# Kernel optimization log

Measured on AMD Instinct MI355X. Metric: run time of the kernel, lower is better.

The kernel has to match this reference:

```python
import jax, jax.numpy as jnp
import numpy as np

QMIN = 0.0
QMAX = 255.0  # uint8, asymmetric


def fake_quant(x, scale, zp):
    # asymmetric uint8 fake-quantization: q = clamp(round(x/s + zp), 0, 255); dq = (q - zp) * s
    s = scale.reshape(())
    z = zp.reshape(())
    q = jnp.clip(jnp.round(x / s + z), QMIN, QMAX)
    return (q - z) * s


def setup_inputs() -> dict:
    key = jax.random.key(0)
    k1, k2 = jax.random.split(key)
    B, M, K, N = 4, 2048, 4096, 4096
    x1 = jax.random.normal(k1, (B, M, K), dtype=jnp.float32)
    x2 = jax.random.normal(k2, (B, K, N), dtype=jnp.float32)
    # realistic learned per-tensor scale / zero-point for ~N(0,1) data over uint8 range
    x1_scale = jnp.full((1,), 8.0 / 255.0, dtype=jnp.float32)
    x1_zp = jnp.full((1,), 128.0, dtype=jnp.float32)
    x2_scale = jnp.full((1,), 8.0 / 255.0, dtype=jnp.float32)
    x2_zp = jnp.full((1,), 128.0, dtype=jnp.float32)
    return {"x1": x1, "x2": x2, "x1_scale": x1_scale, "x1_zp": x1_zp,
            "x2_scale": x2_scale, "x2_zp": x2_zp}


def reference(x1, x2, x1_scale, x1_zp, x2_scale, x2_zp):
    q1 = fake_quant(x1, x1_scale, x1_zp)  # [B, M, K]
    q2 = fake_quant(x2, x2_scale, x2_zp)  # [B, K, N]
    return jnp.matmul(q1, q2)             # [B, M, N]
```

## Files before the change

### kernel.cpp

```cpp
#include <hip/hip_runtime.h>
#include <stdint.h>

typedef int v4i __attribute__((ext_vector_type(4)));

#define GLOBAL_AS __attribute__((address_space(1)))
#define LDS_AS __attribute__((address_space(3)))

__device__ __forceinline__ int quant1(float x, float s, float z, int zi) {
    float q = rintf(x / s + z);
    q = fminf(fmaxf(q, 0.0f), 255.0f);
    return (int)q - zi;
}

__device__ __forceinline__ unsigned qpack4(float4 v, float s, float z, int zi) {
    unsigned q0 = (unsigned)(quant1(v.x, s, z, zi) & 255);
    unsigned q1 = (unsigned)(quant1(v.y, s, z, zi) & 255);
    unsigned q2 = (unsigned)(quant1(v.z, s, z, zi) & 255);
    unsigned q3 = (unsigned)(quant1(v.w, s, z, zi) & 255);
    return q0 | (q1 << 8) | (q2 << 16) | (q3 << 24);
}

__global__ __launch_bounds__(256) void quant_lin(const float* __restrict__ x,
                                                 int8_t* __restrict__ out,
                                                 const float* __restrict__ sp,
                                                 const float* __restrict__ zp,
                                                 long n16) {
    float s = sp[0], z = zp[0];
    int zi = (int)rintf(z);
    long i = (long)blockIdx.x * 256 + threadIdx.x;
    if (i >= n16) return;
    const float4* xv = (const float4*)x;
    uint4 w;
    w.x = qpack4(xv[i * 4 + 0], s, z, zi);
    w.y = qpack4(xv[i * 4 + 1], s, z, zi);
    w.z = qpack4(xv[i * 4 + 2], s, z, zi);
    w.w = qpack4(xv[i * 4 + 3], s, z, zi);
    ((uint4*)out)[i] = w;
}

__global__ __launch_bounds__(256) void quant_bt(const float* __restrict__ x,
                                                int8_t* __restrict__ out,
                                                const float* __restrict__ sp,
                                                const float* __restrict__ zp) {
    constexpr int K = 4096, N = 4096;
    float s = sp[0], z = zp[0];
    int zi = (int)rintf(z);
    size_t bin = (size_t)blockIdx.z * K * N;
    int tid = threadIdx.x;
    int bk = tid >> 4;
    int bn = tid & 15;
    int k0 = blockIdx.y * 64, n0 = blockIdx.x * 64;
    __shared__ unsigned lds[64][17];
    unsigned o0 = 0, o1 = 0, o2 = 0, o3 = 0;
#pragma unroll
    for (int r = 0; r < 4; ++r) {
        float4 v = *(const float4*)(x + bin + (size_t)(k0 + bk * 4 + r) * N + n0 + bn * 4);
        o0 |= (unsigned)(quant1(v.x, s, z, zi) & 255) << (r * 8);
        o1 |= (unsigned)(quant1(v.y, s, z, zi) & 255) << (r * 8);
        o2 |= (unsigned)(quant1(v.z, s, z, zi) & 255) << (r * 8);
        o3 |= (unsigned)(quant1(v.w, s, z, zi) & 255) << (r * 8);
    }
    lds[bn * 4 + 0][bk] = o0;
    lds[bn * 4 + 1][bk] = o1;
    lds[bn * 4 + 2][bk] = o2;
    lds[bn * 4 + 3][bk] = o3;
    __syncthreads();
    int nl = tid >> 2, ch = tid & 3;
    uint4 w;
    w.x = lds[nl][ch * 4 + 0];
    w.y = lds[nl][ch * 4 + 1];
    w.z = lds[nl][ch * 4 + 2];
    w.w = lds[nl][ch * 4 + 3];
    *(uint4*)(out + bin + (size_t)(n0 + nl) * K + k0 + ch * 16) = w;
}

__global__ __launch_bounds__(512, 1) void gemm_i8(const int8_t* __restrict__ A,
                                                  const int8_t* __restrict__ Bt,
                                                  float* __restrict__ C,
                                                  const float* __restrict__ sp1,
                                                  const float* __restrict__ sp2) {
    constexpr int M = 2048, N = 4096, K = 4096;
    constexpr int BM = 256, BN = 256, BK = 64;
    constexpr int NBN = N / BN;

    extern __shared__ char smem[];

    int b = blockIdx.z;
    const int8_t* Ab = A + (size_t)b * M * K;
    const int8_t* Bb = Bt + (size_t)b * N * K;
    float* Cb = C + (size_t)b * M * N;

    int nwg = gridDim.x;
    int wg = blockIdx.x;
    wg = (wg & 7) * (nwg >> 3) + (wg >> 3);
    int by = wg / NBN, bx = wg % NBN;
    int m0 = by * BM, n0 = bx * BN;

    int tid = threadIdx.x;
    int lane = tid & 63, wid = tid >> 6;
    int wr = wid >> 2, wc = wid & 3;
    int l15 = lane & 15, cb = lane >> 4;

    int row0 = tid >> 2, cc0 = tid & 3;
    int sw0 = cc0 ^ ((row0 >> 1) & 3);
    const size_t PSTEP = (size_t)128 * K;
    const int8_t* pA = Ab + (size_t)(m0 + row0) * K + sw0 * 16;
    const int8_t* pB = Bb + (size_t)(n0 + row0) * K + sw0 * 16;
    const unsigned dbase = (unsigned)tid * 16;

    int ra = wr * 128 + l15;
    int aoff0 = ra * 64 + ((cb ^ ((ra >> 1) & 3)) * 16);
    int rb_ = wc * 64 + l15;
    int boff0 = 16384 + rb_ * 64 + ((cb ^ ((rb_ >> 1) & 3)) * 16);

    v4i zero = {0, 0, 0, 0};
    v4i acc[8][4];
#pragma unroll
    for (int m = 0; m < 8; ++m)
#pragma unroll
        for (int n = 0; n < 4; ++n) acc[m][n] = zero;

    v4i fA0[8], fB0[4], fA1[8], fB1[4];

#define ISSUE(S)                                                                        \
    {                                                                                   \
        char* d = smem + (S)*32768 + dbase;                                             \
        __builtin_amdgcn_global_load_lds((const GLOBAL_AS void*)pA,                     \
                                         (LDS_AS void*)d, 16, 0, 0);                    \
        __builtin_amdgcn_global_load_lds((const GLOBAL_AS void*)(pA + PSTEP),           \
                                         (LDS_AS void*)(d + 8192), 16, 0, 0);           \
        __builtin_amdgcn_global_load_lds((const GLOBAL_AS void*)pB,                     \
                                         (LDS_AS void*)(d + 16384), 16, 0, 0);          \
        __builtin_amdgcn_global_load_lds((const GLOBAL_AS void*)(pB + PSTEP),           \
                                         (LDS_AS void*)(d + 24576), 16, 0, 0);          \
        pA += BK;                                                                       \
        pB += BK;                                                                       \
    }

#define RD(S, fa, fb)                                                                   \
    {                                                                                   \
        const char* rbp = smem + (S)*32768;                                             \
        _Pragma("unroll") for (int n = 0; n < 4; ++n)                                   \
            fb[n] = *(const v4i*)(rbp + boff0 + n * 1024);                              \
        _Pragma("unroll") for (int m = 0; m < 8; ++m)                                   \
            fa[m] = *(const v4i*)(rbp + aoff0 + m * 1024);                              \
    }

#define MM(fa, fb)                                                                      \
    {                                                                                   \
        __builtin_amdgcn_s_setprio(1);                                                  \
        _Pragma("unroll") for (int m = 0; m < 8; ++m)                                   \
            _Pragma("unroll") for (int n = 0; n < 4; ++n)                               \
                acc[m][n] = __builtin_amdgcn_mfma_i32_16x16x64_i8(fa[m], fb[n],         \
                                                                  acc[m][n], 0, 0, 0);  \
        __builtin_amdgcn_s_setprio(0);                                                  \
    }

#define SGB3()                                                                          \
    __builtin_amdgcn_sched_group_barrier(0x30, 4, 0);                                   \
    __builtin_amdgcn_sched_group_barrier(0x100, 12, 0);                                 \
    __builtin_amdgcn_sched_group_barrier(0x8, 32, 0);

#define STEP(SI, SR, CA, CB, NA, NB)                                                    \
    {                                                                                   \
        ISSUE(SI);                                                                      \
        RD(SR, NA, NB);                                                                 \
        MM(CA, CB);                                                                     \
        SGB3();                                                                         \
        asm volatile("s_waitcnt vmcnt(4)" ::: "memory");                                \
        __builtin_amdgcn_s_barrier();                                                   \
        asm volatile("" ::: "memory");                                                  \
    }

    ISSUE(0);
    ISSUE(1);
    ISSUE(2);
    asm volatile("s_waitcnt vmcnt(4)" ::: "memory");
    __builtin_amdgcn_s_barrier();
    asm volatile("" ::: "memory");
    RD(0, fA0, fB0);

    for (int it = 0; it < 15; ++it) {
        STEP(3, 1, fA0, fB0, fA1, fB1)
        STEP(0, 2, fA1, fB1, fA0, fB0)
        STEP(1, 3, fA0, fB0, fA1, fB1)
        STEP(2, 0, fA1, fB1, fA0, fB0)
    }
    STEP(3, 1, fA0, fB0, fA1, fB1)
    {
        RD(2, fA0, fB0);
        MM(fA1, fB1);
        asm volatile("s_waitcnt vmcnt(0)" ::: "memory");
        __builtin_amdgcn_s_barrier();
        asm volatile("" ::: "memory");
    }
    RD(3, fA1, fB1);
    MM(fA0, fB0);
    MM(fA1, fB1);

    float sc = sp1[0] * sp2[0];
    int r0 = cb * 4;
#pragma unroll
    for (int m = 0; m < 8; ++m) {
#pragma unroll
        for (int n = 0; n < 4; ++n) {
            float* p = Cb + (size_t)(m0 + wr * 128 + m * 16 + r0) * N +
                       (n0 + wc * 64 + n * 16 + l15);
#pragma unroll
            for (int r = 0; r < 4; ++r) p[(size_t)r * N] = sc * (float)acc[m][n][r];
        }
    }
#undef ISSUE
#undef RD
#undef MM
#undef SGB3
#undef STEP
}

extern "C" void kernel_launch(void* const* d_in, const int* in_sizes, int n_in,
                              void* d_out, int out_size, void* d_ws, size_t ws_size,
                              hipStream_t stream) {
    const float* x1 = (const float*)d_in[0];
    const float* x2 = (const float*)d_in[1];
    const float* s1 = (const float*)d_in[2];
    const float* z1 = (const float*)d_in[3];
    const float* s2 = (const float*)d_in[4];
    const float* z2 = (const float*)d_in[5];
    float* out = (float*)d_out;

    const int B = 4, M = 2048, K = 4096, N = 4096;
    const size_t ASZ = (size_t)B * M * K;
    const size_t BSZ = (size_t)B * K * N;
    dim3 blk(256);

    static int lds_attr_set = 0;
    if (!lds_attr_set) {
        (void)hipFuncSetAttribute((const void*)gemm_i8,
                                  hipFuncAttributeMaxDynamicSharedMemorySize, 131072);
        lds_attr_set = 1;
    }

    if (ws_size >= ASZ + BSZ) {
        int8_t* Aq = (int8_t*)d_ws;
        int8_t* Bq = Aq + ASZ;
        long n16 = (long)(ASZ / 16);
        quant_lin<<<dim3((unsigned)(n16 / 256)), blk, 0, stream>>>(x1, Aq, s1, z1, n16);
        quant_bt<<<dim3(N / 64, K / 64, B), blk, 0, stream>>>(x2, Bq, s2, z2);
        gemm_i8<<<dim3((M / 256) * (N / 256), 1, B), dim3(512), 131072, stream>>>(
            Aq, Bq, out, s1, s2);
    } else {
        const size_t AB = (size_t)M * K, BB = (size_t)K * N;
        int8_t* Aq = (int8_t*)d_ws;
        int8_t* Bq = Aq + AB;
        for (int b = 0; b < B; ++b) {
            long n16 = (long)(AB / 16);
            quant_lin<<<dim3((unsigned)(n16 / 256)), blk, 0, stream>>>(x1 + (size_t)b * AB, Aq, s1, z1, n16);
            quant_bt<<<dim3(N / 64, K / 64, 1), blk, 0, stream>>>(x2 + (size_t)b * BB, Bq, s2, z2);
            gemm_i8<<<dim3((M / 256) * (N / 256), 1, 1), dim3(512), 131072, stream>>>(
                Aq, Bq, out + (size_t)b * M * N, s1, s2);
        }
    }
}
```

Baseline: 250.2 us.

## Deepen GEMM pipeline to five LDS stages and remap grid for XCD locality

The int8 GEMM grows from four to five LDS buffers (160 KB of dynamic LDS), so one more global load stage is in flight, and the wait threshold rises to keep two stages outstanding. The main loop is restructured into a 10-step unrolled cycle with a matching drain sequence. The batched launch becomes a flat 512-block grid whose mapping gives each XCD a contiguous region of one batch, to improve L2 reuse of A and B tiles. The deeper pipeline is meant to hide memory latency better, at the cost of extra LDS and more complex stage indexing.

```diff
diff --git a/kernel.cpp b/kernel.cpp
--- a/kernel.cpp
+++ b/kernel.cpp
@@ -85,15 +85,28 @@
 
     extern __shared__ char smem[];
 
-    int b = blockIdx.z;
+    int b, by, bx;
+    if (gridDim.x == 512) {
+        int p = blockIdx.x;
+        int xcd = p & 7;
+        int q = p >> 3;
+        int round = q >> 5;
+        int s = q & 31;
+        b = round * 2 + (xcd >> 2);
+        int xl = xcd & 3;
+        by = xl * 2 + (s >> 4);
+        bx = s & 15;
+    } else {
+        int nwg = gridDim.x;
+        int wg = blockIdx.x;
+        wg = (wg & 7) * (nwg >> 3) + (wg >> 3);
+        b = blockIdx.z;
+        by = wg / NBN;
+        bx = wg % NBN;
+    }
     const int8_t* Ab = A + (size_t)b * M * K;
     const int8_t* Bb = Bt + (size_t)b * N * K;
     float* Cb = C + (size_t)b * M * N;
-
-    int nwg = gridDim.x;
-    int wg = blockIdx.x;
-    wg = (wg & 7) * (nwg >> 3) + (wg >> 3);
-    int by = wg / NBN, bx = wg % NBN;
     int m0 = by * BM, n0 = bx * BN;
 
     int tid = threadIdx.x;
@@ -161,38 +174,48 @@
     __builtin_amdgcn_sched_group_barrier(0x100, 12, 0);                                 \
     __builtin_amdgcn_sched_group_barrier(0x8, 32, 0);
 
+#define WAITBAR(NW)                                                                     \
+    asm volatile("s_waitcnt vmcnt(" #NW ")" ::: "memory");                              \
+    __builtin_amdgcn_s_barrier();                                                       \
+    asm volatile("" ::: "memory");
+
 #define STEP(SI, SR, CA, CB, NA, NB)                                                    \
     {                                                                                   \
         ISSUE(SI);                                                                      \
         RD(SR, NA, NB);                                                                 \
         MM(CA, CB);                                                                     \
         SGB3();                                                                         \
-        asm volatile("s_waitcnt vmcnt(4)" ::: "memory");                                \
-        __builtin_amdgcn_s_barrier();                                                   \
-        asm volatile("" ::: "memory");                                                  \
+        WAITBAR(8)                                                                      \
     }
 
     ISSUE(0);
     ISSUE(1);
     ISSUE(2);
-    asm volatile("s_waitcnt vmcnt(4)" ::: "memory");
-    __builtin_amdgcn_s_barrier();
-    asm volatile("" ::: "memory");
+    ISSUE(3);
+    WAITBAR(8)
     RD(0, fA0, fB0);
 
-    for (int it = 0; it < 15; ++it) {
-        STEP(3, 1, fA0, fB0, fA1, fB1)
+    for (int it = 0; it < 6; ++it) {
+        STEP(4, 1, fA0, fB0, fA1, fB1)
         STEP(0, 2, fA1, fB1, fA0, fB0)
         STEP(1, 3, fA0, fB0, fA1, fB1)
-        STEP(2, 0, fA1, fB1, fA0, fB0)
-    }
-    STEP(3, 1, fA0, fB0, fA1, fB1)
+        STEP(2, 4, fA1, fB1, fA0, fB0)
+        STEP(3, 0, fA0, fB0, fA1, fB1)
+        STEP(4, 1, fA1, fB1, fA0, fB0)
+        STEP(0, 2, fA0, fB0, fA1, fB1)
+        STEP(1, 3, fA1, fB1, fA0, fB0)
+        STEP(2, 4, fA0, fB0, fA1, fB1)
+        STEP(3, 0, fA1, fB1, fA0, fB0)
+    }
+    {
+        RD(1, fA1, fB1);
+        MM(fA0, fB0);
+        WAITBAR(4)
+    }
     {
         RD(2, fA0, fB0);
         MM(fA1, fB1);
-        asm volatile("s_waitcnt vmcnt(0)" ::: "memory");
-        __builtin_amdgcn_s_barrier();
-        asm volatile("" ::: "memory");
+        WAITBAR(0)
     }
     RD(3, fA1, fB1);
     MM(fA0, fB0);
@@ -214,6 +237,7 @@
 #undef RD
 #undef MM
 #undef SGB3
+#undef WAITBAR
 #undef STEP
 }
 
@@ -236,7 +260,7 @@
     static int lds_attr_set = 0;
     if (!lds_attr_set) {
         (void)hipFuncSetAttribute((const void*)gemm_i8,
-                                  hipFuncAttributeMaxDynamicSharedMemorySize, 131072);
+                                  hipFuncAttributeMaxDynamicSharedMemorySize, 163840);
         lds_attr_set = 1;
     }
 
@@ -246,8 +270,7 @@
         long n16 = (long)(ASZ / 16);
         quant_lin<<<dim3((unsigned)(n16 / 256)), blk, 0, stream>>>(x1, Aq, s1, z1, n16);
         quant_bt<<<dim3(N / 64, K / 64, B), blk, 0, stream>>>(x2, Bq, s2, z2);
-        gemm_i8<<<dim3((M / 256) * (N / 256), 1, B), dim3(512), 131072, stream>>>(
-            Aq, Bq, out, s1, s2);
+        gemm_i8<<<dim3(512, 1, 1), dim3(512), 163840, stream>>>(Aq, Bq, out, s1, s2);
     } else {
         const size_t AB = (size_t)M * K, BB = (size_t)K * N;
         int8_t* Aq = (int8_t*)d_ws;
@@ -256,7 +279,7 @@
             long n16 = (long)(AB / 16);
             quant_lin<<<dim3((unsigned)(n16 / 256)), blk, 0, stream>>>(x1 + (size_t)b * AB, Aq, s1, z1, n16);
             quant_bt<<<dim3(N / 64, K / 64, 1), blk, 0, stream>>>(x2 + (size_t)b * BB, Bq, s2, z2);
-            gemm_i8<<<dim3((M / 256) * (N / 256), 1, 1), dim3(512), 131072, stream>>>(
+            gemm_i8<<<dim3((M / 256) * (N / 256), 1, 1), dim3(512), 163840, stream>>>(
                 Aq, Bq, out + (size_t)b * M * N, s1, s2);
         }
     }
```

Result: slower. 270.2 us (+8.0%).

## Load B fragments directly from global into registers, staging only A in LDS

Applied to the files above, without the earlier changes.

The B operand no longer goes through LDS. Each wave loads its B MFMA fragments straight from global memory into registers one step ahead, and only A stays staged through LDS via global_load_lds. This halves LDS use per block (to 64KB) and removes the LDS reads and writes for B. In exchange, each wave fetches its B data separately, so the four wave rows load duplicate B. Those loads are strided 16-byte global reads whose latency must be hidden inside one pipeline step, and the vmcnt wait counts and schedule barriers were retuned to match.

```diff
diff --git a/kernel.cpp b/kernel.cpp
--- a/kernel.cpp
+++ b/kernel.cpp
@@ -105,13 +105,13 @@
     int sw0 = cc0 ^ ((row0 >> 1) & 3);
     const size_t PSTEP = (size_t)128 * K;
     const int8_t* pA = Ab + (size_t)(m0 + row0) * K + sw0 * 16;
-    const int8_t* pB = Bb + (size_t)(n0 + row0) * K + sw0 * 16;
     const unsigned dbase = (unsigned)tid * 16;
 
     int ra = wr * 128 + l15;
     int aoff0 = ra * 64 + ((cb ^ ((ra >> 1) & 3)) * 16);
-    int rb_ = wc * 64 + l15;
-    int boff0 = 16384 + rb_ * 64 + ((cb ^ ((rb_ >> 1) & 3)) * 16);
+
+    const int8_t* pB = Bb + (size_t)(n0 + wc * 64 + l15) * K + cb * 16;
+    const size_t NSTEP = (size_t)16 * K;
 
     v4i zero = {0, 0, 0, 0};
     v4i acc[8][4];
@@ -120,28 +120,28 @@
 #pragma unroll
         for (int n = 0; n < 4; ++n) acc[m][n] = zero;
 
-    v4i fA0[8], fB0[4], fA1[8], fB1[4];
-
-#define ISSUE(S)                                                                        \
-    {                                                                                   \
-        char* d = smem + (S)*32768 + dbase;                                             \
+    v4i fA0[8], fA1[8], fB0[4], fB1[4];
+
+#define ISSUE_A(S)                                                                      \
+    {                                                                                   \
+        char* d = smem + (S)*16384 + dbase;                                             \
         __builtin_amdgcn_global_load_lds((const GLOBAL_AS void*)pA,                     \
                                          (LDS_AS void*)d, 16, 0, 0);                    \
         __builtin_amdgcn_global_load_lds((const GLOBAL_AS void*)(pA + PSTEP),           \
                                          (LDS_AS void*)(d + 8192), 16, 0, 0);           \
-        __builtin_amdgcn_global_load_lds((const GLOBAL_AS void*)pB,                     \
-                                         (LDS_AS void*)(d + 16384), 16, 0, 0);          \
-        __builtin_amdgcn_global_load_lds((const GLOBAL_AS void*)(pB + PSTEP),           \
-                                         (LDS_AS void*)(d + 24576), 16, 0, 0);          \
         pA += BK;                                                                       \
+    }
+
+#define LDB(fb)                                                                         \
+    {                                                                                   \
+        _Pragma("unroll") for (int n = 0; n < 4; ++n)                                   \
+            fb[n] = *(const v4i*)(pB + (size_t)n * NSTEP);                              \
         pB += BK;                                                                       \
     }
 
-#define RD(S, fa, fb)                                                                   \
-    {                                                                                   \
-        const char* rbp = smem + (S)*32768;                                             \
-        _Pragma("unroll") for (int n = 0; n < 4; ++n)                                   \
-            fb[n] = *(const v4i*)(rbp + boff0 + n * 1024);                              \
+#define RDA(S, fa)                                                                      \
+    {                                                                                   \
+        const char* rbp = smem + (S)*16384;                                             \
         _Pragma("unroll") for (int m = 0; m < 8; ++m)                                   \
             fa[m] = *(const v4i*)(rbp + aoff0 + m * 1024);                              \
     }
@@ -157,28 +157,31 @@
     }
 
 #define SGB3()                                                                          \
-    __builtin_amdgcn_sched_group_barrier(0x30, 4, 0);                                   \
-    __builtin_amdgcn_sched_group_barrier(0x100, 12, 0);                                 \
+    __builtin_amdgcn_sched_group_barrier(0x70, 6, 0);                                   \
+    __builtin_amdgcn_sched_group_barrier(0x100, 8, 0);                                  \
     __builtin_amdgcn_sched_group_barrier(0x8, 32, 0);
 
-#define STEP(SI, SR, CA, CB, NA, NB)                                                    \
-    {                                                                                   \
-        ISSUE(SI);                                                                      \
-        RD(SR, NA, NB);                                                                 \
-        MM(CA, CB);                                                                     \
+#define WAITBAR(NW)                                                                     \
+    asm volatile("s_waitcnt vmcnt(" #NW ")" ::: "memory");                              \
+    __builtin_amdgcn_s_barrier();                                                       \
+    asm volatile("" ::: "memory");
+
+#define STEP(SI, SR, CA, CBF, NA, NBF)                                                  \
+    {                                                                                   \
+        LDB(NBF);                                                                       \
+        ISSUE_A(SI);                                                                    \
+        RDA(SR, NA);                                                                    \
+        MM(CA, CBF);                                                                    \
         SGB3();                                                                         \
-        asm volatile("s_waitcnt vmcnt(4)" ::: "memory");                                \
-        __builtin_amdgcn_s_barrier();                                                   \
-        asm volatile("" ::: "memory");                                                  \
-    }
-
-    ISSUE(0);
-    ISSUE(1);
-    ISSUE(2);
-    asm volatile("s_waitcnt vmcnt(4)" ::: "memory");
-    __builtin_amdgcn_s_barrier();
-    asm volatile("" ::: "memory");
-    RD(0, fA0, fB0);
+        WAITBAR(2)                                                                      \
+    }
+
+    ISSUE_A(0);
+    ISSUE_A(1);
+    LDB(fB0);
+    ISSUE_A(2);
+    WAITBAR(2)
+    RDA(0, fA0);
 
     for (int it = 0; it < 15; ++it) {
         STEP(3, 1, fA0, fB0, fA1, fB1)
@@ -188,14 +191,17 @@
     }
     STEP(3, 1, fA0, fB0, fA1, fB1)
     {
-        RD(2, fA0, fB0);
+        LDB(fB0);
+        RDA(2, fA0);
         MM(fA1, fB1);
-        asm volatile("s_waitcnt vmcnt(0)" ::: "memory");
-        __builtin_amdgcn_s_barrier();
-        asm volatile("" ::: "memory");
-    }
-    RD(3, fA1, fB1);
-    MM(fA0, fB0);
+        WAITBAR(0)
+    }
+    {
+        LDB(fB1);
+        RDA(3, fA1);
+        MM(fA0, fB0);
+        WAITBAR(0)
+    }
     MM(fA1, fB1);
 
     float sc = sp1[0] * sp2[0];
@@ -210,10 +216,12 @@
             for (int r = 0; r < 4; ++r) p[(size_t)r * N] = sc * (float)acc[m][n][r];
         }
     }
-#undef ISSUE
-#undef RD
+#undef ISSUE_A
+#undef LDB
+#undef RDA
 #undef MM
 #undef SGB3
+#undef WAITBAR
 #undef STEP
 }
 
@@ -236,7 +244,7 @@
     static int lds_attr_set = 0;
     if (!lds_attr_set) {
         (void)hipFuncSetAttribute((const void*)gemm_i8,
-                                  hipFuncAttributeMaxDynamicSharedMemorySize, 131072);
+                                  hipFuncAttributeMaxDynamicSharedMemorySize, 65536);
         lds_attr_set = 1;
     }
 
@@ -246,7 +254,7 @@
         long n16 = (long)(ASZ / 16);
         quant_lin<<<dim3((unsigned)(n16 / 256)), blk, 0, stream>>>(x1, Aq, s1, z1, n16);
         quant_bt<<<dim3(N / 64, K / 64, B), blk, 0, stream>>>(x2, Bq, s2, z2);
-        gemm_i8<<<dim3((M / 256) * (N / 256), 1, B), dim3(512), 131072, stream>>>(
+        gemm_i8<<<dim3((M / 256) * (N / 256), 1, B), dim3(512), 65536, stream>>>(
             Aq, Bq, out, s1, s2);
     } else {
         const size_t AB = (size_t)M * K, BB = (size_t)K * N;
@@ -256,7 +264,7 @@
             long n16 = (long)(AB / 16);
             quant_lin<<<dim3((unsigned)(n16 / 256)), blk, 0, stream>>>(x1 + (size_t)b * AB, Aq, s1, z1, n16);
             quant_bt<<<dim3(N / 64, K / 64, 1), blk, 0, stream>>>(x2 + (size_t)b * BB, Bq, s2, z2);
-            gemm_i8<<<dim3((M / 256) * (N / 256), 1, 1), dim3(512), 131072, stream>>>(
+            gemm_i8<<<dim3((M / 256) * (N / 256), 1, 1), dim3(512), 65536, stream>>>(
                 Aq, Bq, out + (size_t)b * M * N, s1, s2);
         }
     }
```

Result: slower. 335.2 us (+33.9%).
